# Optimization experiments

Measured on AMD Instinct MI355X. Metric: run time of the kernel, lower is better.

Reference implementation:

```python
import jax, jax.numpy as jnp
import numpy as np

G = 64      # norm_groups
T = 5       # Newton-Schulz iterations
EPS = 1e-5


def setup_inputs() -> dict:
    key = jax.random.key(0)
    weight = jax.random.normal(key, (2048, 18432), dtype=jnp.float32)
    return {"weight": weight}


def reference(weight):
    out_ch = weight.shape[0]
    # Z: [G, c, d] with c = out_ch // G, d = prod(rest)
    Z = weight.reshape(G, out_ch // G, -1)
    Zc = Z - jnp.mean(Z, axis=-1, keepdims=True)
    # S = Zc @ Zc^T : [G, c, c]
    S = jnp.einsum('gcd,ged->gce', Zc, Zc)
    c = S.shape[-1]
    eye = jnp.eye(c, dtype=S.dtype)
    S = S + EPS * eye
    # Frobenius norm per group, keepdim -> [G,1,1]
    norm_S = jnp.sqrt(jnp.sum(S * S, axis=(1, 2), keepdims=True))
    S = S / norm_S
    # Newton-Schulz: B_{t+1} = 1.5*B_t - 0.5 * B_t^3 @ S
    B = jnp.broadcast_to(eye, S.shape)
    for _ in range(T):
        B3 = jnp.matmul(jnp.matmul(B, B), B)
        B = 1.5 * B - 0.5 * jnp.matmul(B3, S)
    W = jnp.matmul(B, Zc) / jnp.sqrt(norm_S)
    return W.reshape(weight.shape)
```

## Files before the change

kernel.cpp:

```cpp
#include <hip/hip_runtime.h>

#define G 64
#define C 32
#define D 18432
#define NCH 16
#define TD (D / NCH)
#define NST (TD / 128)
#define EPS 1e-5f
#define NS_ITERS 5

typedef __attribute__((ext_vector_type(8))) short short8v;
typedef __attribute__((ext_vector_type(4))) float float4v;

__device__ __forceinline__ void split3(float x, unsigned short& h1,
                                       unsigned short& h2, unsigned short& h3) {
    unsigned int u = __float_as_uint(x);
    unsigned int m1 = u & 0xffff0000u;
    float r1 = x - __uint_as_float(m1);
    unsigned int u2 = __float_as_uint(r1);
    unsigned int m2 = u2 & 0xffff0000u;
    float r2 = r1 - __uint_as_float(m2);
    h1 = (unsigned short)(m1 >> 16);
    h2 = (unsigned short)(m2 >> 16);
    h3 = (unsigned short)(__float_as_uint(r2) >> 16);
}

__device__ __forceinline__ void split8(const float4& v0, const float4& v1,
                                       short8v& p1, short8v& p2, short8v& p3,
                                       float& rs) {
    float x[8] = {v0.x, v0.y, v0.z, v0.w, v1.x, v1.y, v1.z, v1.w};
#pragma unroll
    for (int j = 0; j < 8; ++j) {
        unsigned short h1, h2, h3;
        rs += x[j];
        split3(x[j], h1, h2, h3);
        p1[j] = (short)h1; p2[j] = (short)h2; p3[j] = (short)h3;
    }
}

__global__ __launch_bounds__(256) void k1_gram(const float* __restrict__ W,
                                               float* __restrict__ psum,
                                               float* __restrict__ prow) {
    __shared__ float red[4 * 1056 + 4 * C];

    const int ch   = blockIdx.x;
    const int g    = blockIdx.y;
    const int bid  = g * NCH + ch;
    const int tid  = threadIdx.x;
    const int lane = tid & 63;
    const int wave = tid >> 6;

    const int rbase = lane & 15;
    const int koff  = (lane >> 4) * 8;

    const float* Zg   = W + (size_t)g * C * D + (size_t)ch * TD;
    const float* p0   = Zg + (size_t)rbase * D + wave * 32 + koff;
    const float* p1   = p0 + (size_t)16 * D;

    float4v acc[2][2];
#pragma unroll
    for (int a = 0; a < 2; ++a)
#pragma unroll
        for (int b = 0; b < 2; ++b) acc[a][b] = (float4v)0.f;
    float rs0 = 0.f, rs1 = 0.f;

    float4 c00 = *(const float4*)(p0);
    float4 c01 = *(const float4*)(p0 + 4);
    float4 c10 = *(const float4*)(p1);
    float4 c11 = *(const float4*)(p1 + 4);

#pragma unroll
    for (int st = 0; st < NST; ++st) {
        float4 n00, n01, n10, n11;
        if (st + 1 < NST) {
            n00 = *(const float4*)(p0 + (st + 1) * 128);
            n01 = *(const float4*)(p0 + (st + 1) * 128 + 4);
            n10 = *(const float4*)(p1 + (st + 1) * 128);
            n11 = *(const float4*)(p1 + (st + 1) * 128 + 4);
        }
        short8v fa[3], fb[3];
        split8(c00, c01, fa[0], fa[1], fa[2], rs0);
        split8(c10, c11, fb[0], fb[1], fb[2], rs1);

        short8v* fr[2] = {fa, fb};
#pragma unroll
        for (int a = 0; a < 2; ++a)
#pragma unroll
            for (int b = 0; b < 2; ++b) {
                float4v t = acc[a][b];
                t = __builtin_amdgcn_mfma_f32_16x16x32_bf16(fr[a][0], fr[b][0], t, 0, 0, 0);
                t = __builtin_amdgcn_mfma_f32_16x16x32_bf16(fr[a][0], fr[b][1], t, 0, 0, 0);
                t = __builtin_amdgcn_mfma_f32_16x16x32_bf16(fr[a][1], fr[b][0], t, 0, 0, 0);
                t = __builtin_amdgcn_mfma_f32_16x16x32_bf16(fr[a][1], fr[b][1], t, 0, 0, 0);
                t = __builtin_amdgcn_mfma_f32_16x16x32_bf16(fr[a][0], fr[b][2], t, 0, 0, 0);
                t = __builtin_amdgcn_mfma_f32_16x16x32_bf16(fr[a][2], fr[b][0], t, 0, 0, 0);
                acc[a][b] = t;
            }
        c00 = n00; c01 = n01; c10 = n10; c11 = n11;
    }

    rs0 += __shfl_xor(rs0, 16, 64); rs0 += __shfl_xor(rs0, 32, 64);
    rs1 += __shfl_xor(rs1, 16, 64); rs1 += __shfl_xor(rs1, 32, 64);
    if (lane < 16) {
        red[4224 + wave * C + lane]      = rs0;
        red[4224 + wave * C + 16 + lane] = rs1;
    }

#pragma unroll
    for (int a = 0; a < 2; ++a)
#pragma unroll
        for (int b = 0; b < 2; ++b)
#pragma unroll
            for (int j = 0; j < 4; ++j) {
                int row = 16 * a + ((lane >> 4) << 2) + j;
                int col = 16 * b + (lane & 15);
                red[wave * 1056 + row * 33 + col] = acc[a][b][j];
            }
    __syncthreads();

#pragma unroll
    for (int k = 0; k < 4; ++k) {
        int el = tid + 256 * k;
        int row = el >> 5, col = el & 31;
        int o = row * 33 + col;
        float sv = red[o] + red[1056 + o] + red[2112 + o] + red[3168 + o];
        psum[(size_t)bid * (C * C) + el] = sv;
    }
    if (tid < C) {
        float s = red[4224 + tid] + red[4224 + C + tid] +
                  red[4224 + 2 * C + tid] + red[4224 + 3 * C + tid];
        prow[(size_t)bid * C + tid] = s;
    }
}

__global__ __launch_bounds__(256) void k2_ns(const float* __restrict__ psum,
                                             const float* __restrict__ prow,
                                             float* __restrict__ MT,
                                             float* __restrict__ vout) {
    __shared__ float S[C][C + 1];
    __shared__ float B[C][C + 1];
    __shared__ float T1[C][C + 1];
    __shared__ float T2[C][C + 1];
    __shared__ float mean[C];
    __shared__ float redw[4];
    __shared__ float normsh;

    const int g   = blockIdx.x;
    const int tid = threadIdx.x;
    const int e   = tid & 31;
    const int cbq = tid >> 5;

    float selt[4];
#pragma unroll
    for (int k = 0; k < 4; ++k) {
        int el = tid + 256 * k;
        float s = 0.f;
#pragma unroll
        for (int ch = 0; ch < NCH; ++ch)
            s += psum[((size_t)g * NCH + ch) * (C * C) + el];
        selt[k] = s;
    }
    if (tid < C) {
        float s = 0.f;
#pragma unroll
        for (int ch = 0; ch < NCH; ++ch)
            s += prow[((size_t)g * NCH + ch) * C + tid];
        mean[tid] = s / (float)D;
    }
    __syncthreads();

    float ss = 0.f;
#pragma unroll
    for (int k = 0; k < 4; ++k) {
        int el = tid + 256 * k;
        int c = el >> 5;
        float sv = selt[k] - (float)D * mean[c] * mean[e];
        if (c == e) sv += EPS;
        S[c][e] = sv;
        ss = fmaf(sv, sv, ss);
    }
#pragma unroll
    for (int off = 32; off >= 1; off >>= 1) ss += __shfl_xor(ss, off, 64);
    if ((tid & 63) == 0) redw[tid >> 6] = ss;
    __syncthreads();
    if (tid == 0) normsh = sqrtf(redw[0] + redw[1] + redw[2] + redw[3]);
    __syncthreads();
    const float inv_norm = 1.0f / normsh;
#pragma unroll
    for (int k = 0; k < 4; ++k) {
        int c = cbq + 8 * k;
        S[c][e] *= inv_norm;
        B[c][e] = (c == e) ? 1.f : 0.f;
    }
    __syncthreads();

    for (int it = 0; it < NS_ITERS; ++it) {
#pragma unroll
        for (int k = 0; k < 4; ++k) {
            int c = cbq + 8 * k;
            float s = 0.f;
            for (int kk = 0; kk < C; ++kk)
                s = fmaf(B[c][kk], B[kk][e], s);
            T1[c][e] = s;
        }
        __syncthreads();
#pragma unroll
        for (int k = 0; k < 4; ++k) {
            int c = cbq + 8 * k;
            float s = 0.f;
            for (int kk = 0; kk < C; ++kk)
                s = fmaf(T1[c][kk], B[kk][e], s);
            T2[c][e] = s;
        }
        __syncthreads();
        float pv[4];
#pragma unroll
        for (int k = 0; k < 4; ++k) {
            int c = cbq + 8 * k;
            float s = 0.f;
            for (int kk = 0; kk < C; ++kk)
                s = fmaf(T2[c][kk], S[kk][e], s);
            pv[k] = s;
        }
#pragma unroll
        for (int k = 0; k < 4; ++k) {
            int c = cbq + 8 * k;
            B[c][e] = 1.5f * B[c][e] - 0.5f * pv[k];
        }
        __syncthreads();
    }

    const float invs = 1.0f / sqrtf(normsh);
#pragma unroll
    for (int k = 0; k < 4; ++k) {
        int c = cbq + 8 * k;
        MT[(size_t)g * (C * C) + e * C + c] = B[c][e] * invs;
    }
    if (tid < C) {
        float s = 0.f;
        for (int ee = 0; ee < C; ++ee)
            s = fmaf(B[tid][ee] * invs, mean[ee], s);
        vout[(size_t)g * C + tid] = s;
    }
}

__global__ __launch_bounds__(256) void k3_apply(const float* __restrict__ W,
                                                const float* __restrict__ MT,
                                                const float* __restrict__ vv,
                                                float* __restrict__ out) {
    const int blocksPerGroup = D / 512;
    const int g   = blockIdx.x / blocksPerGroup;
    const int cbk = blockIdx.x % blocksPerGroup;
    const int d0  = cbk * 512 + (int)threadIdx.x * 2;
    const float* Zg = W + (size_t)g * C * D + d0;
    const float* Mg = MT + (size_t)g * (C * C);

    float accx[C], accy[C];
#pragma unroll
    for (int r = 0; r < C; ++r) { accx[r] = 0.f; accy[r] = 0.f; }

    for (int e = 0; e < C; ++e) {
        float2 z = *(const float2*)(Zg + (size_t)e * D);
#pragma unroll
        for (int r = 0; r < C; ++r) {
            float m = Mg[e * C + r];
            accx[r] = fmaf(m, z.x, accx[r]);
            accy[r] = fmaf(m, z.y, accy[r]);
        }
    }

    float* Og = out + (size_t)g * C * D + d0;
#pragma unroll
    for (int r = 0; r < C; ++r) {
        float vr = vv[g * C + r];
        float2 o = make_float2(accx[r] - vr, accy[r] - vr);
        *(float2*)(Og + (size_t)r * D) = o;
    }
}

extern "C" void kernel_launch(void* const* d_in, const int* in_sizes, int n_in,
                              void* d_out, int out_size, void* d_ws, size_t ws_size,
                              hipStream_t stream) {
    const float* w = (const float*)d_in[0];
    float* out = (float*)d_out;

    float* psum = (float*)d_ws;
    float* prow = psum + (size_t)(G * NCH) * (C * C);
    float* MT   = prow + (size_t)(G * NCH) * C;
    float* vv   = MT   + (size_t)G * (C * C);

    k1_gram<<<dim3(NCH, G), 256, 0, stream>>>(w, psum, prow);
    k2_ns  <<<G,            256, 0, stream>>>(psum, prow, MT, vv);
    k3_apply<<<G * (D / 512), 256, 0, stream>>>(w, MT, vv, out);
}
```

Baseline: 94.62 us.

## Fuse Newton-Schulz solve into apply kernel, recomputing per block

```diff
diff --git a/kernel.cpp b/kernel.cpp
--- a/kernel.cpp
+++ b/kernel.cpp
@@ -53,9 +53,9 @@
     const int rbase = lane & 15;
     const int koff  = (lane >> 4) * 8;
 
-    const float* Zg   = W + (size_t)g * C * D + (size_t)ch * TD;
-    const float* p0   = Zg + (size_t)rbase * D + wave * 32 + koff;
-    const float* p1   = p0 + (size_t)16 * D;
+    const float* Zg = W + (size_t)g * C * D + (size_t)ch * TD;
+    const float* p0 = Zg + (size_t)rbase * D + wave * 32 + koff;
+    const float* p1 = p0 + (size_t)16 * D;
 
     float4v acc[2][2];
 #pragma unroll
@@ -133,148 +133,150 @@
     }
 }
 
-__global__ __launch_bounds__(256) void k2_ns(const float* __restrict__ psum,
-                                             const float* __restrict__ prow,
-                                             float* __restrict__ MT,
-                                             float* __restrict__ vout) {
-    __shared__ float S[C][C + 1];
-    __shared__ float B[C][C + 1];
-    __shared__ float T1[C][C + 1];
-    __shared__ float T2[C][C + 1];
+__global__ __launch_bounds__(256) void k3_fused(const float* __restrict__ W,
+                                                const float* __restrict__ psum,
+                                                const float* __restrict__ prow,
+                                                float* __restrict__ out) {
+    __shared__ float buf[4 * 1056];
     __shared__ float mean[C];
     __shared__ float redw[4];
     __shared__ float normsh;
 
-    const int g   = blockIdx.x;
+    const int bpg = D / 512;
+    const int g   = blockIdx.x / bpg;
+    const int cbk = blockIdx.x % bpg;
     const int tid = threadIdx.x;
     const int e   = tid & 31;
     const int cbq = tid >> 5;
 
-    float selt[4];
-#pragma unroll
-    for (int k = 0; k < 4; ++k) {
-        int el = tid + 256 * k;
-        float s = 0.f;
-#pragma unroll
-        for (int ch = 0; ch < NCH; ++ch)
-            s += psum[((size_t)g * NCH + ch) * (C * C) + el];
-        selt[k] = s;
-    }
-    if (tid < C) {
-        float s = 0.f;
-#pragma unroll
-        for (int ch = 0; ch < NCH; ++ch)
-            s += prow[((size_t)g * NCH + ch) * C + tid];
-        mean[tid] = s / (float)D;
-    }
-    __syncthreads();
-
-    float ss = 0.f;
-#pragma unroll
-    for (int k = 0; k < 4; ++k) {
-        int el = tid + 256 * k;
-        int c = el >> 5;
-        float sv = selt[k] - (float)D * mean[c] * mean[e];
-        if (c == e) sv += EPS;
-        S[c][e] = sv;
-        ss = fmaf(sv, sv, ss);
-    }
-#pragma unroll
-    for (int off = 32; off >= 1; off >>= 1) ss += __shfl_xor(ss, off, 64);
-    if ((tid & 63) == 0) redw[tid >> 6] = ss;
-    __syncthreads();
-    if (tid == 0) normsh = sqrtf(redw[0] + redw[1] + redw[2] + redw[3]);
-    __syncthreads();
-    const float inv_norm = 1.0f / normsh;
-#pragma unroll
-    for (int k = 0; k < 4; ++k) {
-        int c = cbq + 8 * k;
-        S[c][e] *= inv_norm;
-        B[c][e] = (c == e) ? 1.f : 0.f;
-    }
-    __syncthreads();
-
-    for (int it = 0; it < NS_ITERS; ++it) {
+    float* Sm  = buf;
+    float* Bm  = buf + 1056;
+    float* T1m = buf + 2112;
+    float* T2m = buf + 3168;
+    float* Ml  = T1m;
+    float* vl  = T2m;
+
+    {
+        float selt[4];
+#pragma unroll
+        for (int k = 0; k < 4; ++k) {
+            int el = tid + 256 * k;
+            float s = 0.f;
+#pragma unroll
+            for (int ch = 0; ch < NCH; ++ch)
+                s += psum[((size_t)g * NCH + ch) * (C * C) + el];
+            selt[k] = s;
+        }
+        if (tid < C) {
+            float s = 0.f;
+#pragma unroll
+            for (int ch = 0; ch < NCH; ++ch)
+                s += prow[((size_t)g * NCH + ch) * C + tid];
+            mean[tid] = s / (float)D;
+        }
+        __syncthreads();
+
+        float ss = 0.f;
+#pragma unroll
+        for (int k = 0; k < 4; ++k) {
+            int el = tid + 256 * k;
+            int c = el >> 5;
+            float sv = selt[k] - (float)D * mean[c] * mean[e];
+            if (c == e) sv += EPS;
+            Sm[c * 33 + e] = sv;
+            ss = fmaf(sv, sv, ss);
+        }
+#pragma unroll
+        for (int off = 32; off >= 1; off >>= 1) ss += __shfl_xor(ss, off, 64);
+        if ((tid & 63) == 0) redw[tid >> 6] = ss;
+        __syncthreads();
+        if (tid == 0) normsh = sqrtf(redw[0] + redw[1] + redw[2] + redw[3]);
+        __syncthreads();
+        const float inv_norm = 1.0f / normsh;
 #pragma unroll
         for (int k = 0; k < 4; ++k) {
             int c = cbq + 8 * k;
+            Sm[c * 33 + e] *= inv_norm;
+            Bm[c * 33 + e] = (c == e) ? 1.f : 0.f;
+        }
+        __syncthreads();
+
+        for (int it = 0; it < NS_ITERS; ++it) {
+#pragma unroll
+            for (int k = 0; k < 4; ++k) {
+                int c = cbq + 8 * k;
+                float s = 0.f;
+                for (int kk = 0; kk < C; ++kk)
+                    s = fmaf(Bm[c * 33 + kk], Bm[kk * 33 + e], s);
+                T1m[c * 33 + e] = s;
+            }
+            __syncthreads();
+#pragma unroll
+            for (int k = 0; k < 4; ++k) {
+                int c = cbq + 8 * k;
+                float s = 0.f;
+                for (int kk = 0; kk < C; ++kk)
+                    s = fmaf(T1m[c * 33 + kk], Bm[kk * 33 + e], s);
+                T2m[c * 33 + e] = s;
+            }
+            __syncthreads();
+            float pv[4];
+#pragma unroll
+            for (int k = 0; k < 4; ++k) {
+                int c = cbq + 8 * k;
+                float s = 0.f;
+                for (int kk = 0; kk < C; ++kk)
+                    s = fmaf(T2m[c * 33 + kk], Sm[kk * 33 + e], s);
+                pv[k] = s;
+            }
+#pragma unroll
+            for (int k = 0; k < 4; ++k) {
+                int c = cbq + 8 * k;
+                Bm[c * 33 + e] = 1.5f * Bm[c * 33 + e] - 0.5f * pv[k];
+            }
+            __syncthreads();
+        }
+
+        const float invs = 1.0f / sqrtf(normsh);
+#pragma unroll
+        for (int k = 0; k < 4; ++k) {
+            int c = cbq + 8 * k;
+            Ml[e * C + c] = Bm[c * 33 + e] * invs;
+        }
+        if (tid < C) {
             float s = 0.f;
-            for (int kk = 0; kk < C; ++kk)
-                s = fmaf(B[c][kk], B[kk][e], s);
-            T1[c][e] = s;
-        }
-        __syncthreads();
-#pragma unroll
-        for (int k = 0; k < 4; ++k) {
-            int c = cbq + 8 * k;
-            float s = 0.f;
-            for (int kk = 0; kk < C; ++kk)
-                s = fmaf(T1[c][kk], B[kk][e], s);
-            T2[c][e] = s;
-        }
-        __syncthreads();
-        float pv[4];
-#pragma unroll
-        for (int k = 0; k < 4; ++k) {
-            int c = cbq + 8 * k;
-            float s = 0.f;
-            for (int kk = 0; kk < C; ++kk)
-                s = fmaf(T2[c][kk], S[kk][e], s);
-            pv[k] = s;
-        }
-#pragma unroll
-        for (int k = 0; k < 4; ++k) {
-            int c = cbq + 8 * k;
-            B[c][e] = 1.5f * B[c][e] - 0.5f * pv[k];
-        }
-        __syncthreads();
-    }
-
-    const float invs = 1.0f / sqrtf(normsh);
-#pragma unroll
-    for (int k = 0; k < 4; ++k) {
-        int c = cbq + 8 * k;
-        MT[(size_t)g * (C * C) + e * C + c] = B[c][e] * invs;
-    }
-    if (tid < C) {
-        float s = 0.f;
-        for (int ee = 0; ee < C; ++ee)
-            s = fmaf(B[tid][ee] * invs, mean[ee], s);
-        vout[(size_t)g * C + tid] = s;
-    }
-}
-
-__global__ __launch_bounds__(256) void k3_apply(const float* __restrict__ W,
-                                                const float* __restrict__ MT,
-                                                const float* __restrict__ vv,
-                                                float* __restrict__ out) {
-    const int blocksPerGroup = D / 512;
-    const int g   = blockIdx.x / blocksPerGroup;
-    const int cbk = blockIdx.x % blocksPerGroup;
-    const int d0  = cbk * 512 + (int)threadIdx.x * 2;
-    const float* Zg = W + (size_t)g * C * D + d0;
-    const float* Mg = MT + (size_t)g * (C * C);
-
-    float accx[C], accy[C];
-#pragma unroll
-    for (int r = 0; r < C; ++r) { accx[r] = 0.f; accy[r] = 0.f; }
-
-    for (int e = 0; e < C; ++e) {
-        float2 z = *(const float2*)(Zg + (size_t)e * D);
+            for (int ee = 0; ee < C; ++ee)
+                s = fmaf(Bm[tid * 33 + ee] * invs, mean[ee], s);
+            vl[tid] = s;
+        }
+        __syncthreads();
+    }
+
+    {
+        const int d0 = cbk * 512 + tid * 2;
+        const float* Zg = W + (size_t)g * C * D + d0;
+
+        float accx[C], accy[C];
+#pragma unroll
+        for (int r = 0; r < C; ++r) { accx[r] = 0.f; accy[r] = 0.f; }
+
+        for (int e2 = 0; e2 < C; ++e2) {
+            float2 z = *(const float2*)(Zg + (size_t)e2 * D);
+#pragma unroll
+            for (int r = 0; r < C; ++r) {
+                float m = Ml[e2 * C + r];
+                accx[r] = fmaf(m, z.x, accx[r]);
+                accy[r] = fmaf(m, z.y, accy[r]);
+            }
+        }
+
+        float* Og = out + (size_t)g * C * D + d0;
 #pragma unroll
         for (int r = 0; r < C; ++r) {
-            float m = Mg[e * C + r];
-            accx[r] = fmaf(m, z.x, accx[r]);
-            accy[r] = fmaf(m, z.y, accy[r]);
-        }
-    }
-
-    float* Og = out + (size_t)g * C * D + d0;
-#pragma unroll
-    for (int r = 0; r < C; ++r) {
-        float vr = vv[g * C + r];
-        float2 o = make_float2(accx[r] - vr, accy[r] - vr);
-        *(float2*)(Og + (size_t)r * D) = o;
+            float vr = vl[r];
+            float2 o = make_float2(accx[r] - vr, accy[r] - vr);
+            *(float2*)(Og + (size_t)r * D) = o;
+        }
     }
 }
 
@@ -286,10 +288,7 @@
 
     float* psum = (float*)d_ws;
     float* prow = psum + (size_t)(G * NCH) * (C * C);
-    float* MT   = prow + (size_t)(G * NCH) * C;
-    float* vv   = MT   + (size_t)G * (C * C);
-
-    k1_gram<<<dim3(NCH, G), 256, 0, stream>>>(w, psum, prow);
-    k2_ns  <<<G,            256, 0, stream>>>(psum, prow, MT, vv);
-    k3_apply<<<G * (D / 512), 256, 0, stream>>>(w, MT, vv, out);
-}
+
+    k1_gram <<<dim3(NCH, G), 256, 0, stream>>>(w, psum, prow);
+    k3_fused<<<G * (D / 512), 256, 0, stream>>>(w, psum, prow, out);
+}
```

Result: slower. 188.1 us (+98.8%).
